# Kernel optimization log

Hardware: AMD Instinct MI355X
Metric: run time of the kernel (lower is better)

The kernel has to match this reference:

```python
import jax, jax.numpy as jnp
import numpy as np

H = 512  # hidden_size


def setup_inputs() -> dict:
    key = jax.random.key(0)
    ks = jax.random.split(key, 13)
    B, S, E, V = 64, 2048, 512, 32000
    s = 0.05
    return {
        "word_input": jax.random.randint(ks[0], (B,), 0, V),
        "last_hidden": jax.random.normal(ks[1], (1, B, H), jnp.float32),
        "encoder_outputs": jax.random.normal(ks[2], (S, B, H), jnp.float32),
        "emb": jax.random.normal(ks[3], (V, E), jnp.float32) * s,
        "attn_W": jax.random.normal(ks[4], (H, 2 * H), jnp.float32) * s,
        "attn_b": jax.random.normal(ks[5], (H,), jnp.float32) * s,
        "v": jax.random.normal(ks[6], (H,), jnp.float32) * s,
        "W_ih": jax.random.normal(ks[7], (3 * H, H + E), jnp.float32) * s,
        "W_hh": jax.random.normal(ks[8], (3 * H, H), jnp.float32) * s,
        "b_ih": jax.random.normal(ks[9], (3 * H,), jnp.float32) * s,
        "b_hh": jax.random.normal(ks[10], (3 * H,), jnp.float32) * s,
        "out_W": jax.random.normal(ks[11], (V, 2 * H), jnp.float32) * s,
        "out_b": jax.random.normal(ks[12], (V,), jnp.float32) * s,
    }


def reference(word_input, last_hidden, encoder_outputs, emb, attn_W, attn_b, v,
              W_ih, W_hh, b_ih, b_hh, out_W, out_b):
    # word_input: [B] int; last_hidden: [1,B,H]; encoder_outputs: [S,B,H]
    hid = last_hidden[-1]                       # [B,H]
    enc = jnp.transpose(encoder_outputs, (1, 0, 2))  # [B,S,H]

    # Bahdanau 'concat' attention: tanh(W [h;e] + b) . v  (split W to avoid [B,S,2H])
    Wa, We = attn_W[:, :H], attn_W[:, H:]
    energy = jnp.tanh((hid @ Wa.T)[:, None, :] + jnp.einsum('bsh,kh->bsk', enc, We) + attn_b)
    scores = jnp.einsum('bsk,k->bs', energy, v)       # [B,S]
    attn = jax.nn.softmax(scores, axis=1)             # [B,S]
    context = jnp.einsum('bs,bsh->bh', attn, enc)     # [B,H]

    # GRU step (PyTorch gate layout: r, z, n)
    x = jnp.concatenate([emb[word_input], context], axis=1)  # [B,E+H]
    gi = x @ W_ih.T + b_ih
    gh = hid @ W_hh.T + b_hh
    r = jax.nn.sigmoid(gi[:, :H] + gh[:, :H])
    z = jax.nn.sigmoid(gi[:, H:2 * H] + gh[:, H:2 * H])
    n = jnp.tanh(gi[:, 2 * H:] + r * gh[:, 2 * H:])
    h_new = (1.0 - z) * n + z * hid                   # [B,H]

    logits = jnp.concatenate([h_new, context], axis=1) @ out_W.T + out_b
    output = jax.nn.log_softmax(logits, axis=1)       # [B,V]
    return output, h_new[None]                        # hidden: [1,B,H]
```

## Files before the change

kernel.cpp:

```cpp
#include <hip/hip_runtime.h>
#include <hip/hip_bf16.h>
#include <cstdint>
#include <cstddef>

#define HD 512
#define BB 64
#define SS 2048
#define VV 32000
#define EE 512
#define MM (SS*BB)

typedef __attribute__((ext_vector_type(8))) short bf16x8;
typedef __attribute__((ext_vector_type(4))) float f32x4;

static __device__ __forceinline__ unsigned short f2bf(float f) {
    union { float f; unsigned u; } x; x.f = f;
    unsigned r = x.u + 0x7fffu + ((x.u >> 16) & 1u);
    return (unsigned short)(r >> 16);
}
static __device__ __forceinline__ unsigned pack2(float a, float b) {
    return (unsigned)f2bf(a) | ((unsigned)f2bf(b) << 16);
}
static __device__ __forceinline__ float tanh_fast(float x) {
    float e = __expf(2.f * x);
    return 1.f - 2.f / (e + 1.f);
}
static __device__ __forceinline__ float sigmoid_fast(float x) {
    return 1.f / (1.f + __expf(-x));
}
static __device__ __forceinline__ void gload16(const void* g, void* l) {
    __builtin_amdgcn_global_load_lds(
        (const __attribute__((address_space(1))) void*)g,
        (__attribute__((address_space(3))) void*)l, 16, 0, 0);
}

__global__ void prep_kernel(const float* __restrict__ hid,
                            const float* __restrict__ attn_W,
                            const float* __restrict__ attn_b,
                            float* __restrict__ qc,
                            uint4* __restrict__ WeB4) {
    int i = blockIdx.x * 256 + threadIdx.x;
    int n = i >> 6, b = i & 63;
    const float* hrow = hid + b * HD;
    const float* wrow = attn_W + (size_t)n * (2 * HD);
    float acc = 0.f;
    for (int k = 0; k < HD; k += 4) {
        float4 h4 = *(const float4*)(hrow + k);
        float4 w4 = *(const float4*)(wrow + k);
        acc += h4.x * w4.x + h4.y * w4.y + h4.z * w4.z + h4.w * w4.w;
    }
    qc[b * HD + n] = acc + attn_b[n];
    int col = (i << 3) & 511;
    const float* src = attn_W + (size_t)n * (2 * HD) + HD + col;
    float4 f0 = *(const float4*)(src);
    float4 f1 = *(const float4*)(src + 4);
    uint4 p;
    p.x = pack2(f0.x, f0.y); p.y = pack2(f0.z, f0.w);
    p.z = pack2(f1.x, f1.y); p.w = pack2(f1.z, f1.w);
    WeB4[n * 64 + (col >> 3)] = p;
}

__global__ __launch_bounds__(512, 4) void scores_kernel(
    const float* __restrict__ enc,
    const uint4* __restrict__ WeB4,
    const float* __restrict__ qc,
    const float* __restrict__ vvec,
    float* __restrict__ scores)
{
    __shared__ uint4 Ald[64 * 8];
    __shared__ uint4 Bld[512 * 8];
    __shared__ float red[64][8];

    const int tid = threadIdx.x;
    const int wv = tid >> 6;
    const int lane = tid & 63;
    const int l15 = lane & 15;
    const int l4 = lane >> 4;
    const int m0 = blockIdx.x * 64;

    f32x4 acc[4][4] = {};

    const int arow = tid >> 3;
    const int ac8 = tid & 7;
    const float* aptr = enc + (size_t)(m0 + arow) * HD + ac8 * 8;
    const int aslot = arow * 8 + (ac8 ^ (arow & 7));

    const int brow = wv * 8 + (lane >> 3);
    const int bchunk = (lane & 7) ^ (lane >> 3);
    const char* bg = (const char*)WeB4 + ((size_t)brow * 64 + bchunk) * 16;

    for (int k0 = 0; k0 < HD; k0 += 64) {
        __syncthreads();
        float4 a0 = *(const float4*)(aptr + k0);
        float4 a1 = *(const float4*)(aptr + k0 + 4);
#pragma unroll
        for (int i = 0; i < 8; ++i)
            gload16(bg + (size_t)i * 64 * 64 * 16 + k0 * 2, &Bld[i * 512 + tid]);
        uint4 ap;
        ap.x = pack2(a0.x, a0.y); ap.y = pack2(a0.z, a0.w);
        ap.z = pack2(a1.x, a1.y); ap.w = pack2(a1.z, a1.w);
        Ald[aslot] = ap;
        __syncthreads();

#pragma unroll
        for (int ks = 0; ks < 2; ++ks) {
            const int chunk = ks * 4 + l4;
            bf16x8 af[4], bfr[4];
#pragma unroll
            for (int mi = 0; mi < 4; ++mi) {
                int row = mi * 16 + l15;
                af[mi] = *(const bf16x8*)&Ald[row * 8 + (chunk ^ (row & 7))];
            }
#pragma unroll
            for (int ni = 0; ni < 4; ++ni) {
                int row = wv * 64 + ni * 16 + l15;
                bfr[ni] = *(const bf16x8*)&Bld[row * 8 + (chunk ^ (row & 7))];
            }
#pragma unroll
            for (int mi = 0; mi < 4; ++mi)
#pragma unroll
                for (int ni = 0; ni < 4; ++ni)
                    acc[mi][ni] = __builtin_amdgcn_mfma_f32_16x16x32_bf16(
                        af[mi], bfr[ni], acc[mi][ni], 0, 0, 0);
        }
    }

    float vv[4];
#pragma unroll
    for (int ni = 0; ni < 4; ++ni) vv[ni] = vvec[wv * 64 + ni * 16 + l15];

#pragma unroll
    for (int mi = 0; mi < 4; ++mi) {
#pragma unroll
        for (int r = 0; r < 4; ++r) {
            const int rowl = mi * 16 + l4 * 4 + r;
            float s = 0.f;
#pragma unroll
            for (int ni = 0; ni < 4; ++ni) {
                int n = wv * 64 + ni * 16 + l15;
                float e = acc[mi][ni][r] + qc[rowl * HD + n];
                s += tanh_fast(e) * vv[ni];
            }
#pragma unroll
            for (int msk = 8; msk >= 1; msk >>= 1)
                s += __shfl_xor(s, msk);
            if (l15 == 0) red[rowl][wv] = s;
        }
    }
    __syncthreads();
    if (tid < 64) {
        float t = 0.f;
#pragma unroll
        for (int w = 0; w < 8; ++w) t += red[tid][w];
        scores[m0 + tid] = t;
    }
}

__global__ void softmax_kernel(float* __restrict__ sc) {
    const int b = blockIdx.x;
    const int tid = threadIdx.x;
    __shared__ float sm[256];
    float m = -1e30f;
    for (int s = tid; s < SS; s += 256) m = fmaxf(m, sc[s * BB + b]);
    sm[tid] = m; __syncthreads();
    for (int o = 128; o > 0; o >>= 1) {
        if (tid < o) sm[tid] = fmaxf(sm[tid], sm[tid + o]);
        __syncthreads();
    }
    m = sm[0]; __syncthreads();
    float sum = 0.f;
    for (int s = tid; s < SS; s += 256) {
        float e = __expf(sc[s * BB + b] - m);
        sc[s * BB + b] = e;
        sum += e;
    }
    sm[tid] = sum; __syncthreads();
    for (int o = 128; o > 0; o >>= 1) {
        if (tid < o) sm[tid] += sm[tid + o];
        __syncthreads();
    }
    float inv = 1.f / sm[0];
    for (int s = tid; s < SS; s += 256) sc[s * BB + b] *= inv;
}

__global__ void ctx_kernel(const float* __restrict__ enc,
                           const float* __restrict__ attn,
                           float* __restrict__ part) {
    const int b = blockIdx.x & 63;
    const int chunk = blockIdx.x >> 6;
    const int h0 = threadIdx.x * 2;
    float2 a; a.x = 0.f; a.y = 0.f;
    const int sbase = chunk * 128;
    for (int si = 0; si < 128; ++si) {
        int s = sbase + si;
        float w = attn[s * BB + b];
        float2 e = *(const float2*)(enc + (size_t)(s * BB + b) * HD + h0);
        a.x += w * e.x; a.y += w * e.y;
    }
    *(float2*)(part + (size_t)(chunk * BB + b) * HD + h0) = a;
}

__global__ void gather_reduce_kernel(const float* __restrict__ part,
                                     const int* __restrict__ word,
                                     const float* __restrict__ emb,
                                     float* __restrict__ x,
                                     float* __restrict__ y) {
    const int b = blockIdx.x;
    const int h0 = threadIdx.x * 2;
    float2 a; a.x = 0.f; a.y = 0.f;
    for (int c = 0; c < 16; ++c) {
        float2 p = *(const float2*)(part + (size_t)(c * BB + b) * HD + h0);
        a.x += p.x; a.y += p.y;
    }
    *(float2*)(x + b * 1024 + HD + h0) = a;
    *(float2*)(y + b * 1024 + HD + h0) = a;
    int w = word[b];
    float2 e = *(const float2*)(emb + (size_t)w * EE + h0);
    *(float2*)(x + b * 1024 + h0) = e;
}

__global__ void gates_kernel(const float* __restrict__ x,
                             const float* __restrict__ hid,
                             const float* __restrict__ W_ih,
                             const float* __restrict__ W_hh,
                             const float* __restrict__ b_ih,
                             const float* __restrict__ b_hh,
                             float* __restrict__ gi, float* __restrict__ gh) {
    const int tid = threadIdx.x;
    const int b = tid & 63;
    const int j = blockIdx.x * 4 + (tid >> 6);
    float agi = 0.f, agh = 0.f;
    const float* xr = x + b * 1024;
    const float* wr = W_ih + (size_t)j * 1024;
    for (int k = 0; k < 1024; k += 4) {
        float4 xv = *(const float4*)(xr + k);
        float4 w4 = *(const float4*)(wr + k);
        agi += xv.x * w4.x + xv.y * w4.y + xv.z * w4.z + xv.w * w4.w;
    }
    const float* hr = hid + b * HD;
    const float* wh = W_hh + (size_t)j * HD;
    for (int k = 0; k < HD; k += 4) {
        float4 hv = *(const float4*)(hr + k);
        float4 w4 = *(const float4*)(wh + k);
        agh += hv.x * w4.x + hv.y * w4.y + hv.z * w4.z + hv.w * w4.w;
    }
    gi[b * 1536 + j] = agi + b_ih[j];
    gh[b * 1536 + j] = agh + b_hh[j];
}

__global__ void hnew_kernel(const float* __restrict__ gi,
                            const float* __restrict__ gh,
                            const float* __restrict__ hid,
                            float* __restrict__ out_h,
                            float* __restrict__ y) {
    const int b = blockIdx.x;
    const int h = threadIdx.x;
    float gr = gi[b * 1536 + h] + gh[b * 1536 + h];
    float gz = gi[b * 1536 + 512 + h] + gh[b * 1536 + 512 + h];
    float r = sigmoid_fast(gr);
    float z = sigmoid_fast(gz);
    float n = tanh_fast(gi[b * 1536 + 1024 + h] + r * gh[b * 1536 + 1024 + h]);
    float hn = (1.f - z) * n + z * hid[b * HD + h];
    out_h[b * HD + h] = hn;
    y[b * 1024 + h] = hn;
}

__global__ __launch_bounds__(256, 4) void logits_kernel(
    const float* __restrict__ y,
    const float* __restrict__ out_W,
    const float* __restrict__ out_b,
    float* __restrict__ logits)
{
    __shared__ uint4 Yld[64 * 8];
    __shared__ uint4 Wld[128 * 8];
    const int tid = threadIdx.x;
    const int wv = tid >> 6;
    const int lane = tid & 63;
    const int l15 = lane & 15, l4 = lane >> 4;
    const int n0 = blockIdx.x * 128;

    f32x4 acc[4][2] = {};

    for (int k0 = 0; k0 < 1024; k0 += 64) {
        __syncthreads();
#pragma unroll
        for (int i = 0; i < 2; ++i) {
            int s = tid + i * 256;
            int row = s >> 3, c8 = s & 7;
            const float* p = y + (size_t)row * 1024 + k0 + c8 * 8;
            float4 f0 = *(const float4*)p, f1 = *(const float4*)(p + 4);
            uint4 u;
            u.x = pack2(f0.x, f0.y); u.y = pack2(f0.z, f0.w);
            u.z = pack2(f1.x, f1.y); u.w = pack2(f1.z, f1.w);
            Yld[row * 8 + (c8 ^ (row & 7))] = u;
        }
#pragma unroll
        for (int i = 0; i < 4; ++i) {
            int s = tid + i * 256;
            int row = s >> 3, c8 = s & 7;
            const float* p = out_W + (size_t)(n0 + row) * 1024 + k0 + c8 * 8;
            float4 f0 = *(const float4*)p, f1 = *(const float4*)(p + 4);
            uint4 u;
            u.x = pack2(f0.x, f0.y); u.y = pack2(f0.z, f0.w);
            u.z = pack2(f1.x, f1.y); u.w = pack2(f1.z, f1.w);
            Wld[row * 8 + (c8 ^ (row & 7))] = u;
        }
        __syncthreads();
#pragma unroll
        for (int ks = 0; ks < 2; ++ks) {
            const int chunk = ks * 4 + l4;
            bf16x8 af[4], bfr[2];
#pragma unroll
            for (int mi = 0; mi < 4; ++mi) {
                int row = mi * 16 + l15;
                af[mi] = *(const bf16x8*)&Yld[row * 8 + (chunk ^ (row & 7))];
            }
#pragma unroll
            for (int ni = 0; ni < 2; ++ni) {
                int row = wv * 32 + ni * 16 + l15;
                bfr[ni] = *(const bf16x8*)&Wld[row * 8 + (chunk ^ (row & 7))];
            }
#pragma unroll
            for (int mi = 0; mi < 4; ++mi)
#pragma unroll
                for (int ni = 0; ni < 2; ++ni)
                    acc[mi][ni] = __builtin_amdgcn_mfma_f32_16x16x32_bf16(
                        af[mi], bfr[ni], acc[mi][ni], 0, 0, 0);
        }
    }
#pragma unroll
    for (int mi = 0; mi < 4; ++mi) {
#pragma unroll
        for (int r = 0; r < 4; ++r) {
            const int b = mi * 16 + l4 * 4 + r;
#pragma unroll
            for (int ni = 0; ni < 2; ++ni) {
                int n = n0 + wv * 32 + ni * 16 + l15;
                logits[(size_t)b * VV + n] = acc[mi][ni][r] + out_b[n];
            }
        }
    }
}

__global__ void lsm_kernel(float* __restrict__ logits) {
    const int b = blockIdx.x;
    const int tid = threadIdx.x;
    __shared__ float sm[1024];
    float* row = logits + (size_t)b * VV;
    float m = -1e30f;
    for (int i = tid; i < VV; i += 1024) m = fmaxf(m, row[i]);
    sm[tid] = m; __syncthreads();
    for (int o = 512; o > 0; o >>= 1) {
        if (tid < o) sm[tid] = fmaxf(sm[tid], sm[tid + o]);
        __syncthreads();
    }
    m = sm[0]; __syncthreads();
    float s = 0.f;
    for (int i = tid; i < VV; i += 1024) s += __expf(row[i] - m);
    sm[tid] = s; __syncthreads();
    for (int o = 512; o > 0; o >>= 1) {
        if (tid < o) sm[tid] += sm[tid + o];
        __syncthreads();
    }
    float lse = m + __logf(sm[0]);
    for (int i = tid; i < VV; i += 1024) row[i] -= lse;
}

extern "C" void kernel_launch(void* const* d_in, const int* in_sizes, int n_in,
                              void* d_out, int out_size, void* d_ws, size_t ws_size,
                              hipStream_t stream) {
    (void)in_sizes; (void)n_in; (void)out_size; (void)ws_size;
    const int*   word   = (const int*)d_in[0];
    const float* hid    = (const float*)d_in[1];
    const float* enc    = (const float*)d_in[2];
    const float* emb    = (const float*)d_in[3];
    const float* attn_W = (const float*)d_in[4];
    const float* attn_b = (const float*)d_in[5];
    const float* v      = (const float*)d_in[6];
    const float* W_ih   = (const float*)d_in[7];
    const float* W_hh   = (const float*)d_in[8];
    const float* b_ih   = (const float*)d_in[9];
    const float* b_hh   = (const float*)d_in[10];
    const float* out_W  = (const float*)d_in[11];
    const float* out_b  = (const float*)d_in[12];

    float* out    = (float*)d_out;
    float* logits = out;
    float* out_h  = out + (size_t)BB * VV;

    char* ws = (char*)d_ws;
    float* qc   = (float*)ws;  ws += 64 * 512 * 4;
    uint4* WeB4 = (uint4*)ws;  ws += 512 * 512 * 2;
    float* sc   = (float*)ws;  ws += MM * 4;
    float* part = (float*)ws;  ws += 16 * 64 * 512 * 4;
    float* x    = (float*)ws;  ws += 64 * 1024 * 4;
    float* y    = (float*)ws;  ws += 64 * 1024 * 4;
    float* gi   = (float*)ws;  ws += 64 * 1536 * 4;
    float* gh   = (float*)ws;  ws += 64 * 1536 * 4;

    prep_kernel<<<128, 256, 0, stream>>>(hid, attn_W, attn_b, qc, WeB4);
    scores_kernel<<<MM / 64, 512, 0, stream>>>(enc, WeB4, qc, v, sc);
    softmax_kernel<<<BB, 256, 0, stream>>>(sc);
    ctx_kernel<<<16 * BB, 256, 0, stream>>>(enc, sc, part);
    gather_reduce_kernel<<<BB, 256, 0, stream>>>(part, word, emb, x, y);
    gates_kernel<<<384, 256, 0, stream>>>(x, hid, W_ih, W_hh, b_ih, b_hh, gi, gh);
    hnew_kernel<<<BB, 512, 0, stream>>>(gi, gh, hid, out_h, y);
    logits_kernel<<<VV / 128, 256, 0, stream>>>(y, out_W, out_b, logits);
    lsm_kernel<<<BB, 1024, 0, stream>>>(logits);
}
```

Before: 397.6 us.

## Double-buffer scores and logits GEMMs, widen tiles, store y as bf16

The scores kernel now handles 128 rows per block, double-buffers the weight tile in LDS and prefetches the next encoder slice into registers, so global loads overlap the MFMA work. The logits kernel keeps the whole bf16 activation matrix in LDS and prefetches out_W two steps ahead. The y activations are written once as bf16 instead of being re-converted from fp32 in every logits block, and ctx/gather/hnew are vectorised to float4 or two elements per thread. The cost is more registers and LDS per block, lower occupancy, and hand-placed waitcnt and barrier logic that must be exactly right.

```diff
diff --git a/kernel.cpp b/kernel.cpp
--- a/kernel.cpp
+++ b/kernel.cpp
@@ -7,7 +7,6 @@
 #define BB 64
 #define SS 2048
 #define VV 32000
-#define EE 512
 #define MM (SS*BB)
 
 typedef __attribute__((ext_vector_type(8))) short bf16x8;
@@ -60,77 +59,103 @@
     WeB4[n * 64 + (col >> 3)] = p;
 }
 
-__global__ __launch_bounds__(512, 4) void scores_kernel(
+__global__ __launch_bounds__(512, 2) void scores_kernel(
     const float* __restrict__ enc,
     const uint4* __restrict__ WeB4,
     const float* __restrict__ qc,
     const float* __restrict__ vvec,
     float* __restrict__ scores)
 {
-    __shared__ uint4 Ald[64 * 8];
-    __shared__ uint4 Bld[512 * 8];
-    __shared__ float red[64][8];
+    __shared__ uint4 Ald[128 * 8];
+    __shared__ uint4 Bld[2][512 * 8];
+    __shared__ float red[128][8];
 
     const int tid = threadIdx.x;
-    const int wv = tid >> 6;
-    const int lane = tid & 63;
-    const int l15 = lane & 15;
-    const int l4 = lane >> 4;
-    const int m0 = blockIdx.x * 64;
-
-    f32x4 acc[4][4] = {};
-
-    const int arow = tid >> 3;
+    const int wv = tid >> 6, lane = tid & 63, l15 = lane & 15, l4 = lane >> 4;
+    const int m0 = blockIdx.x * 128;
+
+    f32x4 acc[8][4] = {};
+
+    const int ar = tid >> 3;
     const int ac8 = tid & 7;
-    const float* aptr = enc + (size_t)(m0 + arow) * HD + ac8 * 8;
-    const int aslot = arow * 8 + (ac8 ^ (arow & 7));
+    const float* ap0 = enc + (size_t)(m0 + ar) * HD + ac8 * 8;
+    const float* ap1 = enc + (size_t)(m0 + 64 + ar) * HD + ac8 * 8;
+    const int asl0 = ar * 8 + (ac8 ^ (ar & 7));
+    const int asl1 = (64 + ar) * 8 + (ac8 ^ (ar & 7));
 
     const int brow = wv * 8 + (lane >> 3);
     const int bchunk = (lane & 7) ^ (lane >> 3);
     const char* bg = (const char*)WeB4 + ((size_t)brow * 64 + bchunk) * 16;
 
-    for (int k0 = 0; k0 < HD; k0 += 64) {
-        __syncthreads();
-        float4 a0 = *(const float4*)(aptr + k0);
-        float4 a1 = *(const float4*)(aptr + k0 + 4);
-#pragma unroll
-        for (int i = 0; i < 8; ++i)
-            gload16(bg + (size_t)i * 64 * 64 * 16 + k0 * 2, &Bld[i * 512 + tid]);
-        uint4 ap;
-        ap.x = pack2(a0.x, a0.y); ap.y = pack2(a0.z, a0.w);
-        ap.z = pack2(a1.x, a1.y); ap.w = pack2(a1.z, a1.w);
-        Ald[aslot] = ap;
-        __syncthreads();
+    float4 pa[2][4];
+    pa[0][0] = *(const float4*)(ap0);
+    pa[0][1] = *(const float4*)(ap0 + 4);
+    pa[0][2] = *(const float4*)(ap1);
+    pa[0][3] = *(const float4*)(ap1 + 4);
+#pragma unroll
+    for (int i = 0; i < 8; ++i)
+        gload16(bg + (size_t)i * 65536, &Bld[0][i * 512 + tid]);
+
+#pragma unroll
+    for (int t = 0; t < 8; ++t) {
+        const int cur = t & 1;
+        if (t < 7) {
+            const int k1 = (t + 1) * 64;
+            pa[cur ^ 1][0] = *(const float4*)(ap0 + k1);
+            pa[cur ^ 1][1] = *(const float4*)(ap0 + k1 + 4);
+            pa[cur ^ 1][2] = *(const float4*)(ap1 + k1);
+            pa[cur ^ 1][3] = *(const float4*)(ap1 + k1 + 4);
+#pragma unroll
+            for (int i = 0; i < 8; ++i)
+                gload16(bg + (size_t)i * 65536 + (size_t)k1 * 2,
+                        &Bld[cur ^ 1][i * 512 + tid]);
+        }
+        uint4 u0, u1;
+        u0.x = pack2(pa[cur][0].x, pa[cur][0].y);
+        u0.y = pack2(pa[cur][0].z, pa[cur][0].w);
+        u0.z = pack2(pa[cur][1].x, pa[cur][1].y);
+        u0.w = pack2(pa[cur][1].z, pa[cur][1].w);
+        u1.x = pack2(pa[cur][2].x, pa[cur][2].y);
+        u1.y = pack2(pa[cur][2].z, pa[cur][2].w);
+        u1.z = pack2(pa[cur][3].x, pa[cur][3].y);
+        u1.w = pack2(pa[cur][3].z, pa[cur][3].w);
+        Ald[asl0] = u0;
+        Ald[asl1] = u1;
+        asm volatile("s_waitcnt lgkmcnt(0)" ::: "memory");
+        __builtin_amdgcn_s_barrier();
+        if (t < 7) { asm volatile("s_waitcnt vmcnt(12)" ::: "memory"); }
+        else       { asm volatile("s_waitcnt vmcnt(0)" ::: "memory"); }
+        __builtin_amdgcn_sched_barrier(0);
 
 #pragma unroll
         for (int ks = 0; ks < 2; ++ks) {
             const int chunk = ks * 4 + l4;
-            bf16x8 af[4], bfr[4];
-#pragma unroll
-            for (int mi = 0; mi < 4; ++mi) {
+            bf16x8 af[8], bfr[4];
+#pragma unroll
+            for (int mi = 0; mi < 8; ++mi) {
                 int row = mi * 16 + l15;
                 af[mi] = *(const bf16x8*)&Ald[row * 8 + (chunk ^ (row & 7))];
             }
 #pragma unroll
             for (int ni = 0; ni < 4; ++ni) {
                 int row = wv * 64 + ni * 16 + l15;
-                bfr[ni] = *(const bf16x8*)&Bld[row * 8 + (chunk ^ (row & 7))];
-            }
-#pragma unroll
-            for (int mi = 0; mi < 4; ++mi)
+                bfr[ni] = *(const bf16x8*)&Bld[cur][row * 8 + (chunk ^ (row & 7))];
+            }
+#pragma unroll
+            for (int mi = 0; mi < 8; ++mi)
 #pragma unroll
                 for (int ni = 0; ni < 4; ++ni)
                     acc[mi][ni] = __builtin_amdgcn_mfma_f32_16x16x32_bf16(
                         af[mi], bfr[ni], acc[mi][ni], 0, 0, 0);
         }
+        __builtin_amdgcn_s_barrier();
     }
 
     float vv[4];
 #pragma unroll
     for (int ni = 0; ni < 4; ++ni) vv[ni] = vvec[wv * 64 + ni * 16 + l15];
-
-#pragma unroll
-    for (int mi = 0; mi < 4; ++mi) {
+#pragma unroll
+    for (int mi = 0; mi < 8; ++mi) {
 #pragma unroll
         for (int r = 0; r < 4; ++r) {
             const int rowl = mi * 16 + l4 * 4 + r;
@@ -138,7 +163,7 @@
 #pragma unroll
             for (int ni = 0; ni < 4; ++ni) {
                 int n = wv * 64 + ni * 16 + l15;
-                float e = acc[mi][ni][r] + qc[rowl * HD + n];
+                float e = acc[mi][ni][r] + qc[(rowl & 63) * HD + n];
                 s += tanh_fast(e) * vv[ni];
             }
 #pragma unroll
@@ -148,7 +173,7 @@
         }
     }
     __syncthreads();
-    if (tid < 64) {
+    if (tid < 128) {
         float t = 0.f;
 #pragma unroll
         for (int w = 0; w < 8; ++w) t += red[tid][w];
@@ -188,35 +213,37 @@
                            float* __restrict__ part) {
     const int b = blockIdx.x & 63;
     const int chunk = blockIdx.x >> 6;
-    const int h0 = threadIdx.x * 2;
-    float2 a; a.x = 0.f; a.y = 0.f;
+    const int h0 = threadIdx.x * 4;
+    float4 a = {0.f, 0.f, 0.f, 0.f};
     const int sbase = chunk * 128;
+#pragma unroll 4
     for (int si = 0; si < 128; ++si) {
         int s = sbase + si;
         float w = attn[s * BB + b];
-        float2 e = *(const float2*)(enc + (size_t)(s * BB + b) * HD + h0);
-        a.x += w * e.x; a.y += w * e.y;
-    }
-    *(float2*)(part + (size_t)(chunk * BB + b) * HD + h0) = a;
+        float4 e = *(const float4*)(enc + (size_t)(s * BB + b) * HD + h0);
+        a.x += w * e.x; a.y += w * e.y; a.z += w * e.z; a.w += w * e.w;
+    }
+    *(float4*)(part + (size_t)(chunk * BB + b) * HD + h0) = a;
 }
 
 __global__ void gather_reduce_kernel(const float* __restrict__ part,
                                      const int* __restrict__ word,
                                      const float* __restrict__ emb,
                                      float* __restrict__ x,
-                                     float* __restrict__ y) {
+                                     unsigned* __restrict__ y_bf) {
     const int b = blockIdx.x;
-    const int h0 = threadIdx.x * 2;
-    float2 a; a.x = 0.f; a.y = 0.f;
+    const int h0 = threadIdx.x * 4;
+    float4 a = {0.f, 0.f, 0.f, 0.f};
     for (int c = 0; c < 16; ++c) {
-        float2 p = *(const float2*)(part + (size_t)(c * BB + b) * HD + h0);
-        a.x += p.x; a.y += p.y;
-    }
-    *(float2*)(x + b * 1024 + HD + h0) = a;
-    *(float2*)(y + b * 1024 + HD + h0) = a;
+        float4 p = *(const float4*)(part + (size_t)(c * BB + b) * HD + h0);
+        a.x += p.x; a.y += p.y; a.z += p.z; a.w += p.w;
+    }
+    *(float4*)(x + b * 1024 + HD + h0) = a;
+    uint2 u; u.x = pack2(a.x, a.y); u.y = pack2(a.z, a.w);
+    *(uint2*)(y_bf + b * 512 + 256 + (h0 >> 1)) = u;
     int w = word[b];
-    float2 e = *(const float2*)(emb + (size_t)w * EE + h0);
-    *(float2*)(x + b * 1024 + h0) = e;
+    float4 e = *(const float4*)(emb + (size_t)w * HD + h0);
+    *(float4*)(x + b * 1024 + h0) = e;
 }
 
 __global__ void gates_kernel(const float* __restrict__ x,
@@ -252,73 +279,96 @@
                             const float* __restrict__ gh,
                             const float* __restrict__ hid,
                             float* __restrict__ out_h,
-                            float* __restrict__ y) {
+                            unsigned* __restrict__ y_bf) {
     const int b = blockIdx.x;
-    const int h = threadIdx.x;
-    float gr = gi[b * 1536 + h] + gh[b * 1536 + h];
-    float gz = gi[b * 1536 + 512 + h] + gh[b * 1536 + 512 + h];
-    float r = sigmoid_fast(gr);
-    float z = sigmoid_fast(gz);
-    float n = tanh_fast(gi[b * 1536 + 1024 + h] + r * gh[b * 1536 + 1024 + h]);
-    float hn = (1.f - z) * n + z * hid[b * HD + h];
-    out_h[b * HD + h] = hn;
-    y[b * 1024 + h] = hn;
-}
-
-__global__ __launch_bounds__(256, 4) void logits_kernel(
-    const float* __restrict__ y,
+    const int h = threadIdx.x * 2;
+    float hn[2];
+#pragma unroll
+    for (int j = 0; j < 2; ++j) {
+        int hh = h + j;
+        float r = sigmoid_fast(gi[b * 1536 + hh] + gh[b * 1536 + hh]);
+        float z = sigmoid_fast(gi[b * 1536 + 512 + hh] + gh[b * 1536 + 512 + hh]);
+        float n = tanh_fast(gi[b * 1536 + 1024 + hh] + r * gh[b * 1536 + 1024 + hh]);
+        hn[j] = (1.f - z) * n + z * hid[b * HD + hh];
+        out_h[b * HD + hh] = hn[j];
+    }
+    y_bf[b * 512 + (h >> 1)] = pack2(hn[0], hn[1]);
+}
+
+__global__ __launch_bounds__(256, 2) void logits_kernel(
+    const unsigned short* __restrict__ y_bf,
     const float* __restrict__ out_W,
     const float* __restrict__ out_b,
     float* __restrict__ logits)
 {
-    __shared__ uint4 Yld[64 * 8];
+    __shared__ uint4 Yld[64 * 128];
     __shared__ uint4 Wld[128 * 8];
     const int tid = threadIdx.x;
-    const int wv = tid >> 6;
-    const int lane = tid & 63;
-    const int l15 = lane & 15, l4 = lane >> 4;
+    const int wv = tid >> 6, lane = tid & 63, l15 = lane & 15, l4 = lane >> 4;
     const int n0 = blockIdx.x * 128;
 
     f32x4 acc[4][2] = {};
 
-    for (int k0 = 0; k0 < 1024; k0 += 64) {
-        __syncthreads();
-#pragma unroll
-        for (int i = 0; i < 2; ++i) {
-            int s = tid + i * 256;
-            int row = s >> 3, c8 = s & 7;
-            const float* p = y + (size_t)row * 1024 + k0 + c8 * 8;
-            float4 f0 = *(const float4*)p, f1 = *(const float4*)(p + 4);
+#pragma unroll
+    for (int i = 0; i < 32; ++i) {
+        int s = i * 256 + tid;
+        int yr = s >> 7, yc = s & 127;
+        gload16(y_bf + ((size_t)yr * 1024 + ((size_t)(yc ^ (yr & 7)) << 3)), &Yld[s]);
+    }
+    const int wr = tid >> 3, wc8 = tid & 7;
+    const float* wp0 = out_W + (size_t)(n0 + wr) * 1024 + wc8 * 8;
+    const int wsl = wc8 ^ (wr & 7);
+    float4 pw[2][8];
+#pragma unroll
+    for (int i = 0; i < 4; ++i) {
+        pw[0][i * 2]     = *(const float4*)(wp0 + (size_t)i * 32768);
+        pw[0][i * 2 + 1] = *(const float4*)(wp0 + (size_t)i * 32768 + 4);
+    }
+#pragma unroll
+    for (int i = 0; i < 4; ++i) {
+        pw[1][i * 2]     = *(const float4*)(wp0 + (size_t)i * 32768 + 64);
+        pw[1][i * 2 + 1] = *(const float4*)(wp0 + (size_t)i * 32768 + 68);
+    }
+    asm volatile("s_waitcnt vmcnt(16)" ::: "memory");
+    __builtin_amdgcn_sched_barrier(0);
+    __builtin_amdgcn_s_barrier();
+
+#pragma unroll
+    for (int t = 0; t < 16; ++t) {
+        const int cur = t & 1;
+#pragma unroll
+        for (int i = 0; i < 4; ++i) {
             uint4 u;
-            u.x = pack2(f0.x, f0.y); u.y = pack2(f0.z, f0.w);
-            u.z = pack2(f1.x, f1.y); u.w = pack2(f1.z, f1.w);
-            Yld[row * 8 + (c8 ^ (row & 7))] = u;
-        }
-#pragma unroll
-        for (int i = 0; i < 4; ++i) {
-            int s = tid + i * 256;
-            int row = s >> 3, c8 = s & 7;
-            const float* p = out_W + (size_t)(n0 + row) * 1024 + k0 + c8 * 8;
-            float4 f0 = *(const float4*)p, f1 = *(const float4*)(p + 4);
-            uint4 u;
-            u.x = pack2(f0.x, f0.y); u.y = pack2(f0.z, f0.w);
-            u.z = pack2(f1.x, f1.y); u.w = pack2(f1.z, f1.w);
-            Wld[row * 8 + (c8 ^ (row & 7))] = u;
-        }
-        __syncthreads();
+            u.x = pack2(pw[cur][i * 2].x, pw[cur][i * 2].y);
+            u.y = pack2(pw[cur][i * 2].z, pw[cur][i * 2].w);
+            u.z = pack2(pw[cur][i * 2 + 1].x, pw[cur][i * 2 + 1].y);
+            u.w = pack2(pw[cur][i * 2 + 1].z, pw[cur][i * 2 + 1].w);
+            Wld[(wr + 32 * i) * 8 + wsl] = u;
+        }
+        if (t < 14) {
+            const int k2 = (t + 2) * 64;
+#pragma unroll
+            for (int i = 0; i < 4; ++i) {
+                pw[cur][i * 2]     = *(const float4*)(wp0 + (size_t)i * 32768 + k2);
+                pw[cur][i * 2 + 1] = *(const float4*)(wp0 + (size_t)i * 32768 + k2 + 4);
+            }
+        }
+        asm volatile("s_waitcnt lgkmcnt(0)" ::: "memory");
+        __builtin_amdgcn_s_barrier();
 #pragma unroll
         for (int ks = 0; ks < 2; ++ks) {
-            const int chunk = ks * 4 + l4;
+            const int kc = t * 8 + ks * 4 + l4;
+            const int wc = ks * 4 + l4;
             bf16x8 af[4], bfr[2];
 #pragma unroll
             for (int mi = 0; mi < 4; ++mi) {
                 int row = mi * 16 + l15;
-                af[mi] = *(const bf16x8*)&Yld[row * 8 + (chunk ^ (row & 7))];
+                af[mi] = *(const bf16x8*)&Yld[row * 128 + (kc ^ (row & 7))];
             }
 #pragma unroll
             for (int ni = 0; ni < 2; ++ni) {
                 int row = wv * 32 + ni * 16 + l15;
-                bfr[ni] = *(const bf16x8*)&Wld[row * 8 + (chunk ^ (row & 7))];
+                bfr[ni] = *(const bf16x8*)&Wld[row * 8 + (wc ^ (row & 7))];
             }
 #pragma unroll
             for (int mi = 0; mi < 4; ++mi)
@@ -327,6 +377,7 @@
                     acc[mi][ni] = __builtin_amdgcn_mfma_f32_16x16x32_bf16(
                         af[mi], bfr[ni], acc[mi][ni], 0, 0, 0);
         }
+        __builtin_amdgcn_s_barrier();
     }
 #pragma unroll
     for (int mi = 0; mi < 4; ++mi) {
@@ -389,22 +440,22 @@
     float* out_h  = out + (size_t)BB * VV;
 
     char* ws = (char*)d_ws;
-    float* qc   = (float*)ws;  ws += 64 * 512 * 4;
-    uint4* WeB4 = (uint4*)ws;  ws += 512 * 512 * 2;
-    float* sc   = (float*)ws;  ws += MM * 4;
-    float* part = (float*)ws;  ws += 16 * 64 * 512 * 4;
-    float* x    = (float*)ws;  ws += 64 * 1024 * 4;
-    float* y    = (float*)ws;  ws += 64 * 1024 * 4;
-    float* gi   = (float*)ws;  ws += 64 * 1536 * 4;
-    float* gh   = (float*)ws;  ws += 64 * 1536 * 4;
+    float* qc      = (float*)ws;    ws += 64 * 512 * 4;
+    uint4* WeB4    = (uint4*)ws;    ws += 512 * 512 * 2;
+    float* sc      = (float*)ws;    ws += MM * 4;
+    float* part    = (float*)ws;    ws += 16 * 64 * 512 * 4;
+    float* x       = (float*)ws;    ws += 64 * 1024 * 4;
+    unsigned* y_bf = (unsigned*)ws; ws += 64 * 1024 * 2;
+    float* gi      = (float*)ws;    ws += 64 * 1536 * 4;
+    float* gh      = (float*)ws;    ws += 64 * 1536 * 4;
 
     prep_kernel<<<128, 256, 0, stream>>>(hid, attn_W, attn_b, qc, WeB4);
-    scores_kernel<<<MM / 64, 512, 0, stream>>>(enc, WeB4, qc, v, sc);
+    scores_kernel<<<MM / 128, 512, 0, stream>>>(enc, WeB4, qc, v, sc);
     softmax_kernel<<<BB, 256, 0, stream>>>(sc);
-    ctx_kernel<<<16 * BB, 256, 0, stream>>>(enc, sc, part);
-    gather_reduce_kernel<<<BB, 256, 0, stream>>>(part, word, emb, x, y);
+    ctx_kernel<<<16 * BB, 128, 0, stream>>>(enc, sc, part);
+    gather_reduce_kernel<<<BB, 128, 0, stream>>>(part, word, emb, x, y_bf);
     gates_kernel<<<384, 256, 0, stream>>>(x, hid, W_ih, W_hh, b_ih, b_hh, gi, gh);
-    hnew_kernel<<<BB, 512, 0, stream>>>(gi, gh, hid, out_h, y);
-    logits_kernel<<<VV / 128, 256, 0, stream>>>(y, out_W, out_b, logits);
+    hnew_kernel<<<BB, 256, 0, stream>>>(gi, gh, hid, out_h, y_bf);
+    logits_kernel<<<VV / 128, 256, 0, stream>>>((const unsigned short*)y_bf, out_W, out_b, logits);
     lsm_kernel<<<BB, 1024, 0, stream>>>(logits);
 }
```

Result: slower. 477.5 us (+20.1%).
